# Performance work log

Hardware: AMD Instinct MI355X
Metric: run time of the kernel (lower is better)

## Reference

```python
import jax, jax.numpy as jnp
import numpy as np

UNITS = 1024
N_CLASSES = 41
SUBSAMPLE = 4
KERNEL = 3
FEAT = 256


def setup_inputs() -> dict:
    key = jax.random.key(0)
    ks = jax.random.split(key, 12)
    B, T, F, U, C = 32, 1000, FEAT, UNITS, N_CLASSES
    s = lambda k, shape, sc: jax.random.normal(k, shape, dtype=jnp.float32) * sc
    return {
        "x": jax.random.normal(ks[0], (B, T, F), dtype=jnp.float32),
        # depthwise conv kernel: (width, 1, channels) for WIO with groups=C
        "conv_w": s(ks[1], (KERNEL, 1, F), 0.1),
        "h0_init": s(ks[2], (1, U), 0.05),
        "w0_x": s(ks[3], (F, 3 * U), 1.0 / np.sqrt(F)),
        "w0_h": s(ks[4], (U, 3 * U), 1.0 / np.sqrt(U)),
        "b0": jnp.zeros((2, 3 * U), dtype=jnp.float32),
        "w1_x": s(ks[5], (U, 3 * U), 1.0 / np.sqrt(U)),
        "w1_h": s(ks[6], (U, 3 * U), 1.0 / np.sqrt(U)),
        "b1": jnp.zeros((2, 3 * U), dtype=jnp.float32),
        "dense_w": s(ks[7], (U, C), 1.0 / np.sqrt(U)),
        "dense_b": jnp.zeros((C,), dtype=jnp.float32),
    }


def _depthwise_conv1d(x, w):
    # x: [B, T, C], w: [K, 1, C]; SAME padding, groups = C, relu, no bias
    C = x.shape[-1]
    y = jax.lax.conv_general_dilated(
        x, w, window_strides=(1,), padding="SAME",
        dimension_numbers=("NWC", "WIO", "NWC"), feature_group_count=C)
    return jax.nn.relu(y)


def _gru_layer(x, h0, Wx, Wh, b):
    # Keras GRU v2 (reset_after=True), gate order z, r, h.
    # x: [B, T, F]; h0: [B, U]; Wx: [F, 3U]; Wh: [U, 3U]; b: [2, 3U]
    xproj = jnp.einsum("btf,fg->btg", x, Wx) + b[0]  # [B, T, 3U]
    br = b[1]

    def step(h, xp):
        rec = h @ Wh + br  # [B, 3U]
        xz, xr, xh = jnp.split(xp, 3, axis=-1)
        rz, rr, rh = jnp.split(rec, 3, axis=-1)
        z = jax.nn.sigmoid(xz + rz)
        r = jax.nn.sigmoid(xr + rr)
        hh = jnp.tanh(xh + r * rh)
        hn = z * h + (1.0 - z) * hh
        return hn, hn

    _, ys = jax.lax.scan(step, h0, jnp.swapaxes(xproj, 0, 1))  # [T, B, U]
    return jnp.swapaxes(ys, 0, 1)


def reference(x, conv_w, h0_init, w0_x, w0_h, b0, w1_x, w1_h, b1, dense_w, dense_b):
    B = x.shape[0]
    U = w0_h.shape[0]
    h = _depthwise_conv1d(x, conv_w)
    # layer 0: learned initial state tiled over batch
    h = _gru_layer(h, jnp.tile(h0_init, (B, 1)), w0_x, w0_h, b0)
    # subsample after layer nLayers-2 == 0
    h = h[:, ::SUBSAMPLE, :]
    # layer 1: zero initial state (Keras default when initial_state is None)
    h = _gru_layer(h, jnp.zeros((B, U), dtype=x.dtype), w1_x, w1_h, b1)
    return h @ dense_w + dense_b  # [B, T//4, nClasses]
```

## Files before the change

kernel.cpp:

```cpp
#include <hip/hip_runtime.h>

typedef unsigned int u32;
typedef unsigned long long u64;
typedef unsigned short u16;
typedef __attribute__((ext_vector_type(8))) short short8;
typedef __attribute__((ext_vector_type(4))) float f32x4;
typedef __attribute__((ext_vector_type(4))) unsigned int u32x4;

#define MFMA(a,b,c) __builtin_amdgcn_mfma_f32_16x16x32_bf16((a),(b),(c),0,0,0)
#define ALOAD32(p)    __hip_atomic_load((p), __ATOMIC_RELAXED, __HIP_MEMORY_SCOPE_AGENT)
#define ASTORE32(p,v) __hip_atomic_store((p),(v), __ATOMIC_RELAXED, __HIP_MEMORY_SCOPE_AGENT)

__device__ __forceinline__ float bf2f(u32 b){ union{u32 u; float f;} v; v.u = b<<16; return v.f; }
__device__ __forceinline__ u16 f2bf(float f){ union{float f; u32 u;} v; v.f = f; u32 u = v.u;
  return (u16)((u + 0x7fffu + ((u>>16)&1u)) >> 16); }
__device__ __forceinline__ u32 pack_f(float v){
  u16 hi = f2bf(v); u16 lo = f2bf(v - bf2f(hi)); return (u32)hi | ((u32)lo<<16); }

__device__ __forceinline__ void unpack8(uint4 a, uint4 b, short8& hi, short8& lo){
  u32 w[8] = {a.x,a.y,a.z,a.w,b.x,b.y,b.z,b.w};
#pragma unroll
  for (int j=0;j<8;++j){ hi[j] = (short)(w[j] & 0xffffu); lo[j] = (short)(w[j] >> 16); }
}
__device__ __forceinline__ void unpackh4(u32x4 a, short8& hi){
#pragma unroll
  for (int i=0;i<4;++i){ hi[2*i] = (short)(a[i] & 0xffffu); hi[2*i+1] = (short)(a[i] >> 16); }
}

constexpr size_t OFF_Y    = 0;
constexpr size_t OFF_SUB  = 32768000;
constexpr size_t OFF_W0IH = 65536000;
constexpr size_t OFF_W0IL = 73400320;
constexpr size_t OFF_W1XH = 81264640;
constexpr size_t OFF_W1XL = 87556096;
constexpr size_t OFF_W1HH = 93847552;
constexpr size_t OFF_W1HL = 100139008;
constexpr size_t OFF_HB0  = 106430464;
constexpr size_t OFF_HB1  = 106692608;
constexpr size_t OFF_FL0  = 106954752;
constexpr size_t OFF_FL1  = 106955776;
constexpr size_t WS_NEED  = 106956800;

__global__ void build_frags(const float* __restrict__ W, u16* __restrict__ fhi,
                            u16* __restrict__ flo, int K){
  const int KT = K >> 8;
  size_t total = (size_t)K * 12 * 256;
  for (size_t i = (size_t)blockIdx.x*blockDim.x + threadIdx.x; i < total;
       i += (size_t)gridDim.x*blockDim.x){
    int j = (int)(i & 7); size_t r = i >> 3;
    int c = (int)(r % 12); r /= 12;
    int kseg = (int)(r & 3); r >>= 2;
    int kt = (int)(r % KT); r /= KT;
    int kq = (int)(r & 7); r >>= 3;
    int wg = (int)r;
    int k = kq*(K>>3) + kt*32 + kseg*8 + j;
    int col = (c>>2)*1024 + wg*4 + (c&3);
    float v = W[(size_t)k*3072 + col];
    u16 hi = f2bf(v);
    u16 lo = f2bf(v - bf2f(hi));
    fhi[i] = hi; flo[i] = lo;
  }
}

__global__ void build_w0img(const float* __restrict__ w0x, const float* __restrict__ w0h,
                            u16* __restrict__ imgH, u16* __restrict__ imgL){
  for (size_t i = (size_t)blockIdx.x*blockDim.x + threadIdx.x; i < 64ull*61440ull;
       i += (size_t)gridDim.x*blockDim.x){
    int wid = (int)(i / 61440), e = (int)(i % 61440);
    int e2, colbase; const float* src;
    if      (e < 4096) { e2 = e;         colbase = 0;    src = w0x; }
    else if (e < 8192) { e2 = e - 4096;  colbase = 1024; src = w0x; }
    else if (e < 24576){ e2 = e - 8192;  colbase = 0;    src = w0h; }
    else if (e < 40960){ e2 = e - 24576; colbase = 1024; src = w0h; }
    else if (e < 45056){ e2 = e - 40960; colbase = 2048; src = w0x; }
    else               { e2 = e - 45056; colbase = 2048; src = w0h; }
    int blk = e2 >> 9, r = e2 & 511;
    int kseg = r >> 7, c = (r >> 3) & 15, j = r & 7;
    int k = blk*32 + kseg*8 + j;
    int col = colbase + wid*16 + c;
    float v = src[(size_t)k*3072 + col];
    u16 hi = f2bf(v);
    imgH[i] = hi; imgL[i] = f2bf(v - bf2f(hi));
  }
}

__global__ void init_state(const float* __restrict__ h0, u32* hb0, u32* hb1,
                           int* f0, int* f1){
  int i = blockIdx.x*blockDim.x + threadIdx.x;
  if (i < 256){ f0[i]=0; f1[i]=0; }
  if (i < 16384){
    int p = i & 511;
    u32 v = (u32)f2bf(h0[2*p]) | ((u32)f2bf(h0[2*p+1]) << 16);
    hb0[i] = v;
    hb1[i] = 0u;
  }
}

__global__ void conv_pack(const float* __restrict__ x, const float* __restrict__ cw,
                          u32* __restrict__ yp){
  for (size_t i = (size_t)blockIdx.x*blockDim.x + threadIdx.x; i < 8192000ull;
       i += (size_t)gridDim.x*blockDim.x){
    int f = (int)(i & 255); int b = (int)((i>>8)&31); int t = (int)(i>>13);
    const float* xb = x + ((size_t)b*1000 + t)*256 + f;
    float acc = xb[0]*cw[256+f];
    if (t > 0)   acc += xb[-256]*cw[f];
    if (t < 999) acc += xb[256]*cw[512+f];
    acc = fmaxf(acc, 0.0f);
    yp[i] = pack_f(acc);
  }
}

__global__ __launch_bounds__(512, 1)
void gru16_persist(const u32* __restrict__ xin,
                   const u16* __restrict__ imgH, const u16* __restrict__ imgL,
                   const float* __restrict__ bias,
                   u32* hbuf, int* flags, u32* out_pack)
{
  __shared__ u16 WIMG[61440];
  __shared__ float exch[8*8*66];
  __shared__ float harr[128];
  __shared__ int hready[32];

  const int tid  = threadIdx.x;
  const int wg   = blockIdx.x;
  const int g    = wg >> 6;
  const int wid  = wg & 63;
  const int lane = tid & 63;
  const int wave = tid >> 6;
  const int kq   = wave;
  const int lo16 = lane & 15, hi16 = lane >> 4;
  const int lane_off = hi16*128 + lo16*8;
  const int hsel = (kq >= 4) ? 16 : 0;
  const int srow = lo16 & 7;

  {
    const u64* sH = (const u64*)(imgH + (size_t)wid*61440);
    u64* dH = (u64*)WIMG;
    for (int i = tid; i < 15360; i += 512) dH[i] = sH[i];
    if (tid < 32) hready[tid] = 0;
    if (tid < 128){
      u16 hv = ((const u16*)hbuf)[g*8192 + (tid>>4)*1024 + wid*16 + (tid&15)];
      harr[tid] = bf2f((u32)hv);
    }
  }
  __syncthreads();

  const u16* gLo  = imgL + (size_t)wid*61440;
  const u16* zx_h = &WIMG[kq*512 + lane_off];          const u16* zx_l = gLo + kq*512 + lane_off;
  const u16* rx_h = &WIMG[4096 + kq*512 + lane_off];   const u16* rx_l = gLo + 4096 + kq*512 + lane_off;
  const u16* zh_h = &WIMG[8192 + kq*2048 + lane_off];  const u16* zh_l = gLo + 8192 + kq*2048 + lane_off;
  const u16* rh_h = &WIMG[24576 + kq*2048 + lane_off]; const u16* rh_l = gLo + 24576 + kq*2048 + lane_off;
  const u16* xh_h = &WIMG[40960 + kq*512 + lane_off];  const u16* xh_l = gLo + 40960 + kq*512 + lane_off;
  const u16* hh_h = &WIMG[45056 + kq*2048 + lane_off]; const u16* hh_l = gLo + 45056 + kq*2048 + lane_off;

  const int gs = tid >> 4, gu = tid & 15, eu = wid*16 + gu;
  const float zb  = bias[eu]        + bias[3072 + eu];
  const float rbv = bias[1024 + eu] + bias[4096 + eu];
  const float hxb = bias[2048 + eu];
  const float hrb = bias[5120 + eu];

  for (int t = 0; t < 1000; ++t) {
    const int cur = t & 1, nxt = cur ^ 1;
    f32x4 aZ  = (f32x4){0.f,0.f,0.f,0.f};
    f32x4 aR  = (f32x4){0.f,0.f,0.f,0.f};
    f32x4 aHX = (f32x4){0.f,0.f,0.f,0.f};
    f32x4 aHR = (f32x4){0.f,0.f,0.f,0.f};
    {
      const u32* xr = xin + ((size_t)t*32 + g*8 + srow)*256 + kq*32 + hi16*8;
      uint4 a0 = *(const uint4*)xr;
      uint4 a1 = *(const uint4*)(xr + 4);
      short8 ahi, alo; unpack8(a0, a1, ahi, alo);
      short8 bzh = *(const short8*)zx_h, bzl = *(const short8*)zx_l;
      short8 brh = *(const short8*)rx_h, brl = *(const short8*)rx_l;
      short8 bxh = *(const short8*)xh_h, bxl = *(const short8*)xh_l;
      aZ  = MFMA(ahi,bzh,aZ);  aZ  = MFMA(alo,bzh,aZ);  aZ  = MFMA(ahi,bzl,aZ);
      aR  = MFMA(ahi,brh,aR);  aR  = MFMA(alo,brh,aR);  aR  = MFMA(ahi,brl,aR);
      aHX = MFMA(ahi,bxh,aHX); aHX = MFMA(alo,bxh,aHX); aHX = MFMA(ahi,bxl,aHX);
    }
    if (t > 0) {
      if (wave == 0) {
        int f0;
        do { f0 = ALOAD32(flags + g*64 + (lane & 31)); } while (__all(f0 >= t) == 0);
        asm volatile("" ::: "memory");
        if (lane == 0) ((volatile int*)hready)[0] = t;
      } else if (wave == 1) {
        int f1;
        do { f1 = ALOAD32(flags + g*64 + 32 + (lane & 31)); } while (__all(f1 >= t) == 0);
        asm volatile("" ::: "memory");
        if (lane == 0) ((volatile int*)hready)[16] = t;
      }
      while (((volatile int*)hready)[hsel] < t) { }
      asm volatile("" ::: "memory");
    }
    {
      const u32* hrow = hbuf + cur*16384 + g*4096 + srow*512 + kq*64 + hi16*4;
      u32x4 qa, qb, qc, qd;
      asm volatile(
        "global_load_dwordx4 %0, %4, off sc0 sc1\n\t"
        "global_load_dwordx4 %1, %4, off offset:64 sc0 sc1\n\t"
        "global_load_dwordx4 %2, %4, off offset:128 sc0 sc1\n\t"
        "global_load_dwordx4 %3, %4, off offset:192 sc0 sc1\n\t"
        "s_waitcnt vmcnt(0)"
        : "=&v"(qa), "=&v"(qb), "=&v"(qc), "=&v"(qd)
        : "v"(hrow)
        : "memory");
      short8 ah0, ah1, ah2, ah3;
      unpackh4(qa, ah0); unpackh4(qb, ah1); unpackh4(qc, ah2); unpackh4(qd, ah3);
#pragma unroll
      for (int kt = 0; kt < 4; ++kt){
        short8 ah = (kt==0)?ah0:(kt==1)?ah1:(kt==2)?ah2:ah3;
        short8 bzh = *(const short8*)(zh_h + kt*512), bzl = *(const short8*)(zh_l + kt*512);
        short8 brh = *(const short8*)(rh_h + kt*512), brl = *(const short8*)(rh_l + kt*512);
        short8 bhh = *(const short8*)(hh_h + kt*512), bhl = *(const short8*)(hh_l + kt*512);
        aZ  = MFMA(ah,bzh,aZ);  aZ  = MFMA(ah,bzl,aZ);
        aR  = MFMA(ah,brh,aR);  aR  = MFMA(ah,brl,aR);
        aHR = MFMA(ah,bhh,aHR); aHR = MFMA(ah,bhl,aHR);
      }
    }
    {
      if (hi16 < 2) {
#pragma unroll
        for (int r4 = 0; r4 < 4; ++r4){
          float* e = &exch[(kq*8 + hi16*4 + r4)*66];
          e[lo16]      = aZ[r4];
          e[16 + lo16] = aR[r4];
          e[32 + lo16] = aHX[r4];
          e[48 + lo16] = aHR[r4];
        }
      }
    }
    __syncthreads();
    u32 pk_out = 0;
    if (tid < 128) {
      float zp=0.f, rp=0.f, xh=0.f, rh=0.f;
#pragma unroll
      for (int k8 = 0; k8 < 8; ++k8){
        const float* e = &exch[(k8*8 + gs)*66];
        zp += e[gu]; rp += e[16+gu]; xh += e[32+gu]; rh += e[48+gu];
      }
      float z = 1.f/(1.f + __expf(-(zp + zb)));
      float r = 1.f/(1.f + __expf(-(rp + rbv)));
      float pre = xh + hxb + r*(rh + hrb);
      float ex = __expf(-2.f*fabsf(pre));
      float th = (1.f - ex)/(1.f + ex);
      float hh = copysignf(th, pre);
      float hn = z*harr[tid] + (1.f - z)*hh;
      harr[tid] = hn;
      pk_out = pack_f(hn);
      int pk16 = (int)(pk_out & 0xffffu);
      int prt  = __shfl_xor(pk16, 1);
      if ((tid & 1) == 0) {
        u32 pair = (u32)pk16 | ((u32)prt << 16);
        ASTORE32(hbuf + nxt*16384 + g*4096 + gs*512 + wid*8 + (gu>>1), pair);
      }
    }
    asm volatile("s_waitcnt vmcnt(0)" ::: "memory");
    __syncthreads();
    if (tid == 0)
      ASTORE32(flags + g*64 + wid, t+1);
    if (tid < 128) {
      if ((t & 3) == 0)
        out_pack[((size_t)(t>>2)*32 + g*8 + gs)*1024 + eu] = pk_out;
    }
  }
}

template<int LAYER>
__global__ __launch_bounds__(1024, 1)
void gru_persist(const u32* __restrict__ xin,
                 const u16* __restrict__ wxf_hi, const u16* __restrict__ wxf_lo,
                 const u16* __restrict__ whf_hi, const u16* __restrict__ whf_lo,
                 const float* __restrict__ bias,
                 u32* hbuf, int* flags, u32* out_pack)
{
  constexpr int T   = (LAYER==0) ? 1000 : 250;
  constexpr int KX  = (LAYER==0) ? 256 : 1024;
  constexpr int KTX = KX >> 8;
  __shared__ u16 WxHi[8*KTX*512], WxLo[8*KTX*512];
  __shared__ u16 WhHi[8*4*512],  WhLo[8*4*512];
  __shared__ float exch[8*32*18];
  __shared__ float harr[128];
  __shared__ int hready[32];

  const int tid  = threadIdx.x;
  const int wg   = blockIdx.x;
  const int lane = tid & 63;
  const int wave = tid >> 6;
  const int m    = wave & 1;
  const int kq   = wave >> 1;
  const int u0   = wg * 4;
  const int lo16 = lane & 15, hi16 = lane >> 4;
  const int lane_off = hi16*128 + lo16*8;
  const int hsel = (kq >= 4) ? 16 : 0;

  {
    for (int i = tid; i < 8*KTX*512/4; i += 1024){ ((u64*)WxHi)[i]=0; ((u64*)WxLo)[i]=0; }
    for (int i = tid; i < 8*4*512/4;  i += 1024){ ((u64*)WhHi)[i]=0; ((u64*)WhLo)[i]=0; }
    if (tid < 32) hready[tid] = 0;
  }
  __syncthreads();
  {
    const u16* bx_hi = wxf_hi + (size_t)wg*KX*12;
    const u16* bx_lo = wxf_lo + (size_t)wg*KX*12;
    const u16* bh_hi = whf_hi + (size_t)wg*1024*12;
    const u16* bh_lo = whf_lo + (size_t)wg*1024*12;
    for (int i = tid; i < 8*KTX*48; i += 1024){
      int c = i % 12; int r = i/12; int kseg = r & 3; r >>= 2;
      int kt = r % KTX; int kqq = r / KTX;
      int ldsoff = ((kqq*KTX+kt)*4+kseg)*128 + c*8;
      *(short8*)&WxHi[ldsoff] = *(const short8*)&bx_hi[(size_t)i*8];
      *(short8*)&WxLo[ldsoff] = *(const short8*)&bx_lo[(size_t)i*8];
    }
    for (int i = tid; i < 8*4*48; i += 1024){
      int c = i % 12; int r = i/12; int kseg = r & 3; r >>= 2;
      int kt = r & 3; int kqq = r >> 2;
      int cm = (c < 8) ? c : (c + 4);
      int ldsoff = ((kqq*4+kt)*4+kseg)*128 + cm*8;
      *(short8*)&WhHi[ldsoff] = *(const short8*)&bh_hi[(size_t)i*8];
      *(short8*)&WhLo[ldsoff] = *(const short8*)&bh_lo[(size_t)i*8];
    }
    if (tid < 128){
      u16 hv = ((const u16*)hbuf)[(tid>>2)*1024 + u0 + (tid&3)];
      harr[tid] = bf2f((u32)hv);
    }
  }
  __syncthreads();

  const int eb = tid >> 2, eu_l = tid & 3, eu = u0 + eu_l;
  const float zb  = bias[eu]        + bias[3072 + eu];
  const float rbv = bias[1024 + eu] + bias[4096 + eu];
  const float hxb = bias[2048 + eu];
  const float hrb = bias[5120 + eu];

  for (int t = 0; t < T; ++t) {
    const int cur = t & 1, nxt = cur ^ 1;
    f32x4 xacc = (f32x4){0.f,0.f,0.f,0.f};
    f32x4 racc = (f32x4){0.f,0.f,0.f,0.f};
    {
      const u32* xrow = xin + ((size_t)t*32 + 16*m + lo16)*KX + kq*(KX>>3) + hi16*8;
#pragma unroll
      for (int kt = 0; kt < KTX; ++kt) {
        uint4 a0 = *(const uint4*)(xrow + kt*32);
        uint4 a1 = *(const uint4*)(xrow + kt*32 + 4);
        short8 ahi, alo; unpack8(a0, a1, ahi, alo);
        short8 bhi = *(const short8*)&WxHi[(kq*KTX+kt)*512 + lane_off];
        short8 blo = *(const short8*)&WxLo[(kq*KTX+kt)*512 + lane_off];
        xacc = MFMA(ahi, bhi, xacc);
        xacc = MFMA(alo, bhi, xacc);
        xacc = MFMA(ahi, blo, xacc);
      }
    }
    if (t > 0) {
      if (wave == 0) {
        int f0, f1;
        do { f0 = ALOAD32(flags + lane); f1 = ALOAD32(flags + 64 + lane); }
        while (!__all(f0 >= t && f1 >= t));
        asm volatile("" ::: "memory");
        if (lane == 0) ((volatile int*)hready)[0] = t;
      } else if (wave == 1) {
        int f2, f3;
        do { f2 = ALOAD32(flags + 128 + lane); f3 = ALOAD32(flags + 192 + lane); }
        while (!__all(f2 >= t && f3 >= t));
        asm volatile("" ::: "memory");
        if (lane == 0) ((volatile int*)hready)[16] = t;
      }
      while (((volatile int*)hready)[hsel] < t) { }
      asm volatile("" ::: "memory");
    }
    {
      const u32* hrow = hbuf + cur*16384 + (16*m + lo16)*512 + kq*64 + hi16*4;
      u32x4 qa, qb, qc, qd;
      asm volatile(
        "global_load_dwordx4 %0, %4, off sc0 sc1\n\t"
        "global_load_dwordx4 %1, %4, off offset:64 sc0 sc1\n\t"
        "global_load_dwordx4 %2, %4, off offset:128 sc0 sc1\n\t"
        "global_load_dwordx4 %3, %4, off offset:192 sc0 sc1\n\t"
        "s_waitcnt vmcnt(0)"
        : "=&v"(qa), "=&v"(qb), "=&v"(qc), "=&v"(qd)
        : "v"(hrow)
        : "memory");
      short8 ah0, ah1, ah2, ah3;
      unpackh4(qa, ah0); unpackh4(qb, ah1); unpackh4(qc, ah2); unpackh4(qd, ah3);
      {
        short8 bhi = *(const short8*)&WhHi[(kq*4+0)*512 + lane_off];
        short8 blo = *(const short8*)&WhLo[(kq*4+0)*512 + lane_off];
        racc = MFMA(ah0, bhi, racc); racc = MFMA(ah0, blo, racc);
      }
      {
        short8 bhi = *(const short8*)&WhHi[(kq*4+1)*512 + lane_off];
        short8 blo = *(const short8*)&WhLo[(kq*4+1)*512 + lane_off];
        racc = MFMA(ah1, bhi, racc); racc = MFMA(ah1, blo, racc);
      }
      {
        short8 bhi = *(const short8*)&WhHi[(kq*4+2)*512 + lane_off];
        short8 blo = *(const short8*)&WhLo[(kq*4+2)*512 + lane_off];
        racc = MFMA(ah2, bhi, racc); racc = MFMA(ah2, blo, racc);
      }
      {
        short8 bhi = *(const short8*)&WhHi[(kq*4+3)*512 + lane_off];
        short8 blo = *(const short8*)&WhLo[(kq*4+3)*512 + lane_off];
        racc = MFMA(ah3, bhi, racc); racc = MFMA(ah3, blo, racc);
      }
    }
    {
      const int bb = 16*m + hi16*4;
#pragma unroll
      for (int r4 = 0; r4 < 4; ++r4)
        exch[(kq*32 + bb + r4)*18 + lo16] = xacc[r4] + racc[r4];
    }
    __syncthreads();
    u32 pk_out = 0;
    if (tid < 128) {
      float zp=0.f, rp=0.f, xh=0.f, rh=0.f;
#pragma unroll
      for (int qd = 0; qd < 8; ++qd) {
        const float* e = &exch[(qd*32 + eb)*18];
        zp += e[eu_l];
        rp += e[4 + eu_l];
        xh += e[8 + eu_l];
        rh += e[12 + eu_l];
      }
      float z = 1.f/(1.f + __expf(-(zp + zb)));
      float r = 1.f/(1.f + __expf(-(rp + rbv)));
      float pre = xh + hxb + r*(rh + hrb);
      float ex = __expf(-2.f*fabsf(pre));
      float th = (1.f - ex)/(1.f + ex);
      float hh = copysignf(th, pre);
      float hn = z*harr[tid] + (1.f - z)*hh;
      harr[tid] = hn;
      pk_out = pack_f(hn);
      int pk16 = (int)(pk_out & 0xffffu);
      int prt  = __shfl_xor(pk16, 1);
      if ((tid & 1) == 0) {
        u32 pair = (u32)pk16 | ((u32)prt << 16);
        ASTORE32(hbuf + nxt*16384 + eb*512 + wg*2 + (eu_l>>1), pair);
      }
    }
    asm volatile("s_waitcnt vmcnt(0)" ::: "memory");
    __syncthreads();
    if (tid == 0)
      ASTORE32(flags + wg, t+1);
    if (tid < 128) {
      if (LAYER==0) {
        if ((t & 3) == 0)
          out_pack[((size_t)(t>>2)*32 + eb)*1024 + u0 + eu_l] = pk_out;
      } else {
        out_pack[((size_t)t*32 + eb)*1024 + u0 + eu_l] = pk_out;
      }
    }
  }
}

__global__ __launch_bounds__(256, 1)
void dense_k(const u32* __restrict__ h2, const float* __restrict__ W,
             const float* __restrict__ bias, float* __restrict__ out){
  __shared__ float rows[32*1025];
  const int ts = blockIdx.x;
  const u32* src = h2 + (size_t)ts*32768;
  for (int i = threadIdx.x; i < 32768; i += 256){
    u32 p = src[i];
    rows[(i>>10)*1025 + (i&1023)] = bf2f(p & 0xffffu) + bf2f(p >> 16);
  }
  __syncthreads();
  const int b = threadIdx.x >> 3, cg = threadIdx.x & 7;
  float acc[6] = {0.f,0.f,0.f,0.f,0.f,0.f};
  for (int k = 0; k < 1024; ++k){
    float hv = rows[b*1025 + k];
    const float* wr = W + k*41;
#pragma unroll
    for (int j = 0; j < 6; ++j){ int c = cg + 8*j; if (c < 41) acc[j] += hv*wr[c]; }
  }
#pragma unroll
  for (int j = 0; j < 6; ++j){
    int c = cg + 8*j;
    if (c < 41) out[((size_t)b*250 + ts)*41 + c] = acc[j] + bias[c];
  }
}

extern "C" void kernel_launch(void* const* d_in, const int* in_sizes, int n_in,
                              void* d_out, int out_size, void* d_ws, size_t ws_size,
                              hipStream_t stream) {
  const float* x      = (const float*)d_in[0];
  const float* conv_w = (const float*)d_in[1];
  const float* h0i    = (const float*)d_in[2];
  const float* w0x    = (const float*)d_in[3];
  const float* w0h    = (const float*)d_in[4];
  const float* b0     = (const float*)d_in[5];
  const float* w1x    = (const float*)d_in[6];
  const float* w1h    = (const float*)d_in[7];
  const float* b1     = (const float*)d_in[8];
  const float* dw     = (const float*)d_in[9];
  const float* db     = (const float*)d_in[10];
  float* outp = (float*)d_out;

  if (ws_size < WS_NEED) return;

  char* ws = (char*)d_ws;
  u32* y_pack   = (u32*)(ws + OFF_Y);
  u32* out2     = (u32*)(ws + OFF_Y);
  u32* sub_pack = (u32*)(ws + OFF_SUB);
  u16* w0iH = (u16*)(ws + OFF_W0IH); u16* w0iL = (u16*)(ws + OFF_W0IL);
  u16* w1x_hi = (u16*)(ws + OFF_W1XH); u16* w1x_lo = (u16*)(ws + OFF_W1XL);
  u16* w1h_hi = (u16*)(ws + OFF_W1HH); u16* w1h_lo = (u16*)(ws + OFF_W1HL);
  u32* hb0 = (u32*)(ws + OFF_HB0);
  u32* hb1 = (u32*)(ws + OFF_HB1);
  int* fl0 = (int*)(ws + OFF_FL0);
  int* fl1 = (int*)(ws + OFF_FL1);

  init_state<<<64, 512, 0, stream>>>(h0i, hb0, hb1, fl0, fl1);
  build_w0img<<<2048, 256, 0, stream>>>(w0x, w0h, w0iH, w0iL);
  build_frags<<<2048, 256, 0, stream>>>(w1x, w1x_hi, w1x_lo, 1024);
  build_frags<<<2048, 256, 0, stream>>>(w1h, w1h_hi, w1h_lo, 1024);
  conv_pack<<<4096, 256, 0, stream>>>(x, conv_w, y_pack);

  gru16_persist<<<256, 512, 0, stream>>>(y_pack, w0iH, w0iL, b0, hb0, fl0, sub_pack);
  gru_persist<1><<<256, 1024, 0, stream>>>(sub_pack, w1x_hi, w1x_lo, w1h_hi, w1h_lo,
                                           b1, hb1, fl1, out2);

  dense_k<<<250, 256, 0, stream>>>(out2, dw, db, outp);
}
```

Measured before the change: 5.962 ms.

## Split layer-1 GRU into two batch groups with 8-unit workgroups

Replaces the layer-1 persistent GRU kernel (256 WGs × 1024 threads, each owning 4 units for all 32 batch rows) with one where the batch is split into two 16-row groups of 128 workgroups each. Each 512-thread workgroup owns 8 units, and flag polling is per group, so each group only synchronizes with 128 peers instead of 256. Weights are pre-packed into a per-workgroup image; only the bf16 hi parts sit in LDS while the lo parts are streamed from global memory each step. The intent is to shrink the per-step barrier scope and halve the MFMA M-dimension waste. The cost is extra global weight traffic per step.

```diff
diff --git a/kernel.cpp b/kernel.cpp
--- a/kernel.cpp
+++ b/kernel.cpp
@@ -31,36 +31,13 @@
 constexpr size_t OFF_SUB  = 32768000;
 constexpr size_t OFF_W0IH = 65536000;
 constexpr size_t OFF_W0IL = 73400320;
-constexpr size_t OFF_W1XH = 81264640;
-constexpr size_t OFF_W1XL = 87556096;
-constexpr size_t OFF_W1HH = 93847552;
-constexpr size_t OFF_W1HL = 100139008;
+constexpr size_t OFF_W1IH = 81264640;
+constexpr size_t OFF_W1IL = 93847552;
 constexpr size_t OFF_HB0  = 106430464;
 constexpr size_t OFF_HB1  = 106692608;
 constexpr size_t OFF_FL0  = 106954752;
 constexpr size_t OFF_FL1  = 106955776;
 constexpr size_t WS_NEED  = 106956800;
-
-__global__ void build_frags(const float* __restrict__ W, u16* __restrict__ fhi,
-                            u16* __restrict__ flo, int K){
-  const int KT = K >> 8;
-  size_t total = (size_t)K * 12 * 256;
-  for (size_t i = (size_t)blockIdx.x*blockDim.x + threadIdx.x; i < total;
-       i += (size_t)gridDim.x*blockDim.x){
-    int j = (int)(i & 7); size_t r = i >> 3;
-    int c = (int)(r % 12); r /= 12;
-    int kseg = (int)(r & 3); r >>= 2;
-    int kt = (int)(r % KT); r /= KT;
-    int kq = (int)(r & 7); r >>= 3;
-    int wg = (int)r;
-    int k = kq*(K>>3) + kt*32 + kseg*8 + j;
-    int col = (c>>2)*1024 + wg*4 + (c&3);
-    float v = W[(size_t)k*3072 + col];
-    u16 hi = f2bf(v);
-    u16 lo = f2bf(v - bf2f(hi));
-    fhi[i] = hi; flo[i] = lo;
-  }
-}
 
 __global__ void build_w0img(const float* __restrict__ w0x, const float* __restrict__ w0h,
                             u16* __restrict__ imgH, u16* __restrict__ imgL){
@@ -84,6 +61,25 @@
   }
 }
 
+__global__ void build_w1img(const float* __restrict__ w1x, const float* __restrict__ w1h,
+                            u16* __restrict__ imgH, u16* __restrict__ imgL){
+  for (size_t i = (size_t)blockIdx.x*blockDim.x + threadIdx.x; i < 128ull*49152ull;
+       i += (size_t)gridDim.x*blockDim.x){
+    int wid = (int)(i / 49152), e = (int)(i % 49152);
+    int rg = e >> 14, e2 = e & 16383;
+    int blk = e2 >> 9, rr = e2 & 511;
+    int kseg = rr >> 7, c = (rr >> 3) & 15, j = rr & 7;
+    int k = blk*32 + kseg*8 + j;
+    const float* src; int col;
+    if (rg == 0){ src = w1x; col = (c<8) ? (wid*8+c) : (1024 + wid*8 + c-8); }
+    else if (rg == 1){ src = w1h; col = (c<8) ? (wid*8+c) : (1024 + wid*8 + c-8); }
+    else { col = 2048 + wid*8 + ((c<8) ? c : c-8); src = (c<8) ? w1x : w1h; }
+    float v = src[(size_t)k*3072 + col];
+    u16 hi = f2bf(v);
+    imgH[i] = hi; imgL[i] = f2bf(v - bf2f(hi));
+  }
+}
+
 __global__ void init_state(const float* __restrict__ h0, u32* hb0, u32* hb1,
                            int* f0, int* f1){
   int i = blockIdx.x*blockDim.x + threadIdx.x;
@@ -265,102 +261,78 @@
   }
 }
 
-template<int LAYER>
-__global__ __launch_bounds__(1024, 1)
-void gru_persist(const u32* __restrict__ xin,
-                 const u16* __restrict__ wxf_hi, const u16* __restrict__ wxf_lo,
-                 const u16* __restrict__ whf_hi, const u16* __restrict__ whf_lo,
-                 const float* __restrict__ bias,
-                 u32* hbuf, int* flags, u32* out_pack)
+__global__ __launch_bounds__(512, 1)
+void gru8L1_persist(const u32* __restrict__ xin,
+                    const u16* __restrict__ imgH, const u16* __restrict__ imgL,
+                    const float* __restrict__ bias,
+                    u32* hbuf, int* flags, u32* out_pack)
 {
-  constexpr int T   = (LAYER==0) ? 1000 : 250;
-  constexpr int KX  = (LAYER==0) ? 256 : 1024;
-  constexpr int KTX = KX >> 8;
-  __shared__ u16 WxHi[8*KTX*512], WxLo[8*KTX*512];
-  __shared__ u16 WhHi[8*4*512],  WhLo[8*4*512];
-  __shared__ float exch[8*32*18];
+  __shared__ u16 WIMG[49152];
+  __shared__ float exch[8*16*33];
   __shared__ float harr[128];
   __shared__ int hready[32];
 
   const int tid  = threadIdx.x;
   const int wg   = blockIdx.x;
+  const int g    = wg >> 7;
+  const int wid  = wg & 127;
   const int lane = tid & 63;
   const int wave = tid >> 6;
-  const int m    = wave & 1;
-  const int kq   = wave >> 1;
-  const int u0   = wg * 4;
+  const int kq   = wave;
   const int lo16 = lane & 15, hi16 = lane >> 4;
   const int lane_off = hi16*128 + lo16*8;
   const int hsel = (kq >= 4) ? 16 : 0;
 
   {
-    for (int i = tid; i < 8*KTX*512/4; i += 1024){ ((u64*)WxHi)[i]=0; ((u64*)WxLo)[i]=0; }
-    for (int i = tid; i < 8*4*512/4;  i += 1024){ ((u64*)WhHi)[i]=0; ((u64*)WhLo)[i]=0; }
+    const u64* sH = (const u64*)(imgH + (size_t)wid*49152);
+    u64* dH = (u64*)WIMG;
+    for (int i = tid; i < 12288; i += 512) dH[i] = sH[i];
     if (tid < 32) hready[tid] = 0;
+    if (tid < 128){
+      u16 hv = ((const u16*)hbuf)[g*16384 + (tid>>3)*1024 + wid*8 + (tid&7)];
+      harr[tid] = bf2f((u32)hv);
+    }
   }
   __syncthreads();
-  {
-    const u16* bx_hi = wxf_hi + (size_t)wg*KX*12;
-    const u16* bx_lo = wxf_lo + (size_t)wg*KX*12;
-    const u16* bh_hi = whf_hi + (size_t)wg*1024*12;
-    const u16* bh_lo = whf_lo + (size_t)wg*1024*12;
-    for (int i = tid; i < 8*KTX*48; i += 1024){
-      int c = i % 12; int r = i/12; int kseg = r & 3; r >>= 2;
-      int kt = r % KTX; int kqq = r / KTX;
-      int ldsoff = ((kqq*KTX+kt)*4+kseg)*128 + c*8;
-      *(short8*)&WxHi[ldsoff] = *(const short8*)&bx_hi[(size_t)i*8];
-      *(short8*)&WxLo[ldsoff] = *(const short8*)&bx_lo[(size_t)i*8];
-    }
-    for (int i = tid; i < 8*4*48; i += 1024){
-      int c = i % 12; int r = i/12; int kseg = r & 3; r >>= 2;
-      int kt = r & 3; int kqq = r >> 2;
-      int cm = (c < 8) ? c : (c + 4);
-      int ldsoff = ((kqq*4+kt)*4+kseg)*128 + cm*8;
-      *(short8*)&WhHi[ldsoff] = *(const short8*)&bh_hi[(size_t)i*8];
-      *(short8*)&WhLo[ldsoff] = *(const short8*)&bh_lo[(size_t)i*8];
-    }
-    if (tid < 128){
-      u16 hv = ((const u16*)hbuf)[(tid>>2)*1024 + u0 + (tid&3)];
-      harr[tid] = bf2f((u32)hv);
-    }
-  }
-  __syncthreads();
-
-  const int eb = tid >> 2, eu_l = tid & 3, eu = u0 + eu_l;
+
+  const u16* gLo   = imgL + (size_t)wid*49152;
+  const u16* zrx_h = &WIMG[kq*2048 + lane_off];          const u16* zrx_l = gLo + kq*2048 + lane_off;
+  const u16* zrh_h = &WIMG[16384 + kq*2048 + lane_off];  const u16* zrh_l = gLo + 16384 + kq*2048 + lane_off;
+  const u16* xhh_h = &WIMG[32768 + kq*2048 + lane_off];  const u16* xhh_l = gLo + 32768 + kq*2048 + lane_off;
+
+  const int gs = tid >> 3, gu = tid & 7, eu = wid*8 + gu;
   const float zb  = bias[eu]        + bias[3072 + eu];
   const float rbv = bias[1024 + eu] + bias[4096 + eu];
   const float hxb = bias[2048 + eu];
   const float hrb = bias[5120 + eu];
 
-  for (int t = 0; t < T; ++t) {
+  for (int t = 0; t < 250; ++t) {
     const int cur = t & 1, nxt = cur ^ 1;
-    f32x4 xacc = (f32x4){0.f,0.f,0.f,0.f};
-    f32x4 racc = (f32x4){0.f,0.f,0.f,0.f};
-    {
-      const u32* xrow = xin + ((size_t)t*32 + 16*m + lo16)*KX + kq*(KX>>3) + hi16*8;
-#pragma unroll
-      for (int kt = 0; kt < KTX; ++kt) {
+    f32x4 aZR = (f32x4){0.f,0.f,0.f,0.f};
+    f32x4 aXH = (f32x4){0.f,0.f,0.f,0.f};
+    f32x4 aHR = (f32x4){0.f,0.f,0.f,0.f};
+    {
+      const u32* xrow = xin + ((size_t)t*32 + g*16 + lo16)*1024 + kq*128 + hi16*8;
+#pragma unroll
+      for (int kt = 0; kt < 4; ++kt) {
         uint4 a0 = *(const uint4*)(xrow + kt*32);
         uint4 a1 = *(const uint4*)(xrow + kt*32 + 4);
         short8 ahi, alo; unpack8(a0, a1, ahi, alo);
-        short8 bhi = *(const short8*)&WxHi[(kq*KTX+kt)*512 + lane_off];
-        short8 blo = *(const short8*)&WxLo[(kq*KTX+kt)*512 + lane_off];
-        xacc = MFMA(ahi, bhi, xacc);
-        xacc = MFMA(alo, bhi, xacc);
-        xacc = MFMA(ahi, blo, xacc);
+        short8 bzh = *(const short8*)(zrx_h + kt*512), bzl = *(const short8*)(zrx_l + kt*512);
+        short8 bxh = *(const short8*)(xhh_h + kt*512), bxl = *(const short8*)(xhh_l + kt*512);
+        aZR = MFMA(ahi,bzh,aZR); aZR = MFMA(alo,bzh,aZR); aZR = MFMA(ahi,bzl,aZR);
+        aXH = MFMA(ahi,bxh,aXH); aXH = MFMA(alo,bxh,aXH); aXH = MFMA(ahi,bxl,aXH);
       }
     }
     if (t > 0) {
       if (wave == 0) {
-        int f0, f1;
-        do { f0 = ALOAD32(flags + lane); f1 = ALOAD32(flags + 64 + lane); }
-        while (!__all(f0 >= t && f1 >= t));
+        int f0;
+        do { f0 = ALOAD32(flags + g*128 + lane); } while (__all(f0 >= t) == 0);
         asm volatile("" ::: "memory");
         if (lane == 0) ((volatile int*)hready)[0] = t;
       } else if (wave == 1) {
-        int f2, f3;
-        do { f2 = ALOAD32(flags + 128 + lane); f3 = ALOAD32(flags + 192 + lane); }
-        while (!__all(f2 >= t && f3 >= t));
+        int f1;
+        do { f1 = ALOAD32(flags + g*128 + 64 + lane); } while (__all(f1 >= t) == 0);
         asm volatile("" ::: "memory");
         if (lane == 0) ((volatile int*)hready)[16] = t;
       }
@@ -368,7 +340,7 @@
       asm volatile("" ::: "memory");
     }
     {
-      const u32* hrow = hbuf + cur*16384 + (16*m + lo16)*512 + kq*64 + hi16*4;
+      const u32* hrow = hbuf + cur*16384 + g*8192 + lo16*512 + kq*64 + hi16*4;
       u32x4 qa, qb, qc, qd;
       asm volatile(
         "global_load_dwordx4 %0, %4, off sc0 sc1\n\t"
@@ -381,44 +353,31 @@
         : "memory");
       short8 ah0, ah1, ah2, ah3;
       unpackh4(qa, ah0); unpackh4(qb, ah1); unpackh4(qc, ah2); unpackh4(qd, ah3);
-      {
-        short8 bhi = *(const short8*)&WhHi[(kq*4+0)*512 + lane_off];
-        short8 blo = *(const short8*)&WhLo[(kq*4+0)*512 + lane_off];
-        racc = MFMA(ah0, bhi, racc); racc = MFMA(ah0, blo, racc);
-      }
-      {
-        short8 bhi = *(const short8*)&WhHi[(kq*4+1)*512 + lane_off];
-        short8 blo = *(const short8*)&WhLo[(kq*4+1)*512 + lane_off];
-        racc = MFMA(ah1, bhi, racc); racc = MFMA(ah1, blo, racc);
-      }
-      {
-        short8 bhi = *(const short8*)&WhHi[(kq*4+2)*512 + lane_off];
-        short8 blo = *(const short8*)&WhLo[(kq*4+2)*512 + lane_off];
-        racc = MFMA(ah2, bhi, racc); racc = MFMA(ah2, blo, racc);
-      }
-      {
-        short8 bhi = *(const short8*)&WhHi[(kq*4+3)*512 + lane_off];
-        short8 blo = *(const short8*)&WhLo[(kq*4+3)*512 + lane_off];
-        racc = MFMA(ah3, bhi, racc); racc = MFMA(ah3, blo, racc);
-      }
-    }
-    {
-      const int bb = 16*m + hi16*4;
-#pragma unroll
-      for (int r4 = 0; r4 < 4; ++r4)
-        exch[(kq*32 + bb + r4)*18 + lo16] = xacc[r4] + racc[r4];
+#pragma unroll
+      for (int kt = 0; kt < 4; ++kt){
+        short8 ah = (kt==0)?ah0:(kt==1)?ah1:(kt==2)?ah2:ah3;
+        short8 bzh = *(const short8*)(zrh_h + kt*512), bzl = *(const short8*)(zrh_l + kt*512);
+        short8 bhh = *(const short8*)(xhh_h + kt*512), bhl = *(const short8*)(xhh_l + kt*512);
+        aZR = MFMA(ah,bzh,aZR); aZR = MFMA(ah,bzl,aZR);
+        aHR = MFMA(ah,bhh,aHR); aHR = MFMA(ah,bhl,aHR);
+      }
+    }
+    {
+#pragma unroll
+      for (int r4 = 0; r4 < 4; ++r4){
+        float* e = &exch[(kq*16 + hi16*4 + r4)*33];
+        e[lo16]      = aZR[r4];
+        e[16 + lo16] = (lo16 < 8) ? aXH[r4] : aHR[r4];
+      }
     }
     __syncthreads();
     u32 pk_out = 0;
     if (tid < 128) {
       float zp=0.f, rp=0.f, xh=0.f, rh=0.f;
 #pragma unroll
-      for (int qd = 0; qd < 8; ++qd) {
-        const float* e = &exch[(qd*32 + eb)*18];
-        zp += e[eu_l];
-        rp += e[4 + eu_l];
-        xh += e[8 + eu_l];
-        rh += e[12 + eu_l];
+      for (int k8 = 0; k8 < 8; ++k8){
+        const float* e = &exch[(k8*16 + gs)*33];
+        zp += e[gu]; rp += e[8+gu]; xh += e[16+gu]; rh += e[24+gu];
       }
       float z = 1.f/(1.f + __expf(-(zp + zb)));
       float r = 1.f/(1.f + __expf(-(rp + rbv)));
@@ -433,20 +392,15 @@
       int prt  = __shfl_xor(pk16, 1);
       if ((tid & 1) == 0) {
         u32 pair = (u32)pk16 | ((u32)prt << 16);
-        ASTORE32(hbuf + nxt*16384 + eb*512 + wg*2 + (eu_l>>1), pair);
+        ASTORE32(hbuf + nxt*16384 + g*8192 + gs*512 + wid*4 + (gu>>1), pair);
       }
     }
     asm volatile("s_waitcnt vmcnt(0)" ::: "memory");
     __syncthreads();
     if (tid == 0)
-      ASTORE32(flags + wg, t+1);
+      ASTORE32(flags + g*128 + wid, t+1);
     if (tid < 128) {
-      if (LAYER==0) {
-        if ((t & 3) == 0)
-          out_pack[((size_t)(t>>2)*32 + eb)*1024 + u0 + eu_l] = pk_out;
-      } else {
-        out_pack[((size_t)t*32 + eb)*1024 + u0 + eu_l] = pk_out;
-      }
+      out_pack[((size_t)t*32 + g*16 + gs)*1024 + eu] = pk_out;
     }
   }
 }
@@ -500,8 +454,7 @@
   u32* out2     = (u32*)(ws + OFF_Y);
   u32* sub_pack = (u32*)(ws + OFF_SUB);
   u16* w0iH = (u16*)(ws + OFF_W0IH); u16* w0iL = (u16*)(ws + OFF_W0IL);
-  u16* w1x_hi = (u16*)(ws + OFF_W1XH); u16* w1x_lo = (u16*)(ws + OFF_W1XL);
-  u16* w1h_hi = (u16*)(ws + OFF_W1HH); u16* w1h_lo = (u16*)(ws + OFF_W1HL);
+  u16* w1iH = (u16*)(ws + OFF_W1IH); u16* w1iL = (u16*)(ws + OFF_W1IL);
   u32* hb0 = (u32*)(ws + OFF_HB0);
   u32* hb1 = (u32*)(ws + OFF_HB1);
   int* fl0 = (int*)(ws + OFF_FL0);
@@ -509,13 +462,11 @@
 
   init_state<<<64, 512, 0, stream>>>(h0i, hb0, hb1, fl0, fl1);
   build_w0img<<<2048, 256, 0, stream>>>(w0x, w0h, w0iH, w0iL);
-  build_frags<<<2048, 256, 0, stream>>>(w1x, w1x_hi, w1x_lo, 1024);
-  build_frags<<<2048, 256, 0, stream>>>(w1h, w1h_hi, w1h_lo, 1024);
+  build_w1img<<<2048, 256, 0, stream>>>(w1x, w1h, w1iH, w1iL);
   conv_pack<<<4096, 256, 0, stream>>>(x, conv_w, y_pack);
 
   gru16_persist<<<256, 512, 0, stream>>>(y_pack, w0iH, w0iL, b0, hb0, fl0, sub_pack);
-  gru_persist<1><<<256, 1024, 0, stream>>>(sub_pack, w1x_hi, w1x_lo, w1h_hi, w1h_lo,
-                                           b1, hb1, fl1, out2);
+  gru8L1_persist<<<256, 512, 0, stream>>>(sub_pack, w1iH, w1iL, b1, hb1, fl1, out2);
 
   dense_k<<<250, 256, 0, stream>>>(out2, dw, db, outp);
 }
```

Result: faster. 5.423 ms, median of 2 (-9.0%).
